# Kernel tuning notes

Measured on AMD Instinct MI355X. Metric: run time of the kernel, lower is better.

## Reference

```python
import jax, jax.numpy as jnp
import numpy as np


def _mlp(h, weights, biases, n_relu):
    # Linear(+ReLU) stack; ReLU on the first n_relu layers, final layer linear only.
    for i, (w, b) in enumerate(zip(weights, biases)):
        h = h @ w + b
        if i < n_relu:
            h = jax.nn.relu(h)
    return h


def setup_inputs() -> dict:
    key = jax.random.key(0)
    ks = jax.random.split(key, 12)
    B, M, E = 16384, 512, 1024

    def lin(k, fan_in, fan_out):
        # xavier-ish scaling so activations stay well-conditioned
        return jax.random.normal(k, (fan_in, fan_out), jnp.float32) * (1.0 / np.sqrt(fan_in))

    return {
        "x": jax.random.normal(ks[0], (B, M), jnp.float32),
        "rand_noise": jax.random.uniform(ks[1], (B, M), jnp.float32),
        "u_random": jax.random.uniform(ks[2], (B, M), jnp.float32),
        "marginals_min": jnp.zeros((M,), jnp.float32),
        "marginals_max": jnp.ones((M,), jnp.float32),
        "enc_w0": lin(ks[3], M, E), "enc_b0": jnp.full((E,), 0.01, jnp.float32),
        "enc_w1": lin(ks[4], E, E), "enc_b1": jnp.full((E,), 0.01, jnp.float32),
        "enc_w2": lin(ks[5], E, E), "enc_b2": jnp.full((E,), 0.01, jnp.float32),
        "enc_w3": lin(ks[6], E, E), "enc_b3": jnp.full((E,), 0.01, jnp.float32),
        "head_w0": lin(ks[7], E, E), "head_b0": jnp.full((E,), 0.01, jnp.float32),
        "head_w1": lin(ks[8], E, E), "head_b1": jnp.full((E,), 0.01, jnp.float32),
        "corruption_len": 307,
    }


def reference(x, rand_noise, u_random, marginals_min, marginals_max,
              enc_w0, enc_b0, enc_w1, enc_b1, enc_w2, enc_b2, enc_w3, enc_b3,
              head_w0, head_b0, head_w1, head_b1, corruption_len):
    B, M = x.shape
    # Vectorized equivalent of per-row randperm(m)[:corruption_len]:
    # top-k of iid uniform noise picks a uniform random subset of size k per row.
    _, idx = jax.lax.top_k(rand_noise, corruption_len)            # [B, k]
    mask = jnp.zeros((B, M), bool).at[jnp.arange(B)[:, None], idx].set(True)

    # Marginal samples ~ Uniform(min, max) per feature.
    x_random = marginals_min + u_random * (marginals_max - marginals_min)
    x_corrupted = jnp.where(mask, x_random, x)

    enc_ws = [enc_w0, enc_w1, enc_w2, enc_w3]
    enc_bs = [enc_b0, enc_b1, enc_b2, enc_b3]
    head_ws = [head_w0, head_w1]
    head_bs = [head_b0, head_b1]

    # Run both branches through one batched pass (same math, fewer launches).
    both = jnp.concatenate([x, x_corrupted], axis=0)              # [2B, M]
    h = _mlp(both, enc_ws, enc_bs, n_relu=3)                      # encoder depth 4
    h = _mlp(h, head_ws, head_bs, n_relu=1)                       # head depth 2
    embeddings, embeddings_corrupted = h[:B], h[B:]
    return embeddings, embeddings_corrupted
```

## Files before the change

### kernel.cpp

```cpp
#include <hip/hip_runtime.h>

typedef _Float16 f16x8 __attribute__((ext_vector_type(8)));
typedef float f32x4 __attribute__((ext_vector_type(4)));

__device__ __forceinline__ void gload16(const void* g, void* l) {
  __builtin_amdgcn_global_load_lds(
      (const __attribute__((address_space(1))) void*)g,
      (__attribute__((address_space(3))) void*)l, 16, 0, 0);
}

__device__ __forceinline__ void barfence() {
  asm volatile("" ::: "memory");
  __builtin_amdgcn_s_barrier();
  asm volatile("" ::: "memory");
}

__device__ __forceinline__ int xcd_swz(int orig, int nwg) {
  int q = nwg >> 3, r = nwg & 7;
  int x = orig & 7, loc = orig >> 3;
  int base = (x < r) ? x * (q + 1) : r * (q + 1) + (x - r) * q;
  return base + loc;
}

struct WPtrs { const float* w[6]; _Float16* wt[6]; };
__global__ __launch_bounds__(256) void transpose_all(WPtrs p) {
  const int N = 1024;
  __shared__ float tile[32][33];
  int y = blockIdx.y, layer, ky;
  if (y < 16) { layer = 0; ky = y; }
  else { int t = y - 16; layer = 1 + (t >> 5); ky = t & 31; }
  int K = (layer == 0) ? 512 : 1024;
  const float* W = p.w[layer];
  _Float16* WT = p.wt[layer];
  int tx = threadIdx.x, ty = threadIdx.y;
  int n0 = blockIdx.x * 32, k0 = ky * 32;
#pragma unroll
  for (int i = 0; i < 4; i++)
    tile[ty + i * 8][tx] = W[(long)(k0 + ty + i * 8) * N + (n0 + tx)];
  __syncthreads();
#pragma unroll
  for (int i = 0; i < 4; i++)
    WT[(long)(n0 + ty + i * 8) * K + (k0 + tx)] = (_Float16)tile[tx][ty + i * 8];
}

__global__ __launch_bounds__(256) void cast_f16(const float* __restrict__ in,
                                                _Float16* __restrict__ out, long n) {
  long i = ((long)blockIdx.x * 256 + threadIdx.x) * 4;
  if (i < n) {
    float4 v = *(const float4*)(in + i);
    typedef _Float16 f16x4 __attribute__((ext_vector_type(4)));
    f16x4 o = {(_Float16)v.x, (_Float16)v.y, (_Float16)v.z, (_Float16)v.w};
    *(f16x4*)(out + i) = o;
  }
}

__global__ __launch_bounds__(256) void topk_corrupt(
    const float* __restrict__ noise, const float* __restrict__ x,
    const float* __restrict__ u, const float* __restrict__ mmin,
    const float* __restrict__ mmax, const int* __restrict__ kptr,
    _Float16* __restrict__ dplain, _Float16* __restrict__ dcorr,
    int xrow0, int nrows) {
  int lane = threadIdx.x & 63;
  int r = (blockIdx.x << 2) + (threadIdx.x >> 6);
  if (r >= nrows) return;
  long row = (long)xrow0 + r;
  long rb = row * 512 + lane * 8;
  float4 n0 = *(const float4*)(noise + rb);
  float4 n1 = *(const float4*)(noise + rb + 4);
  unsigned v[8] = {__float_as_uint(n0.x), __float_as_uint(n0.y),
                   __float_as_uint(n0.z), __float_as_uint(n0.w),
                   __float_as_uint(n1.x), __float_as_uint(n1.y),
                   __float_as_uint(n1.z), __float_as_uint(n1.w)};
  int kk = *kptr;
  unsigned T = 0;
  for (int bit = 30; bit >= 0; --bit) {
    unsigned Tp = T | (1u << bit);
    int c = 0;
#pragma unroll
    for (int j = 0; j < 8; j++) c += (int)__popcll(__ballot(v[j] >= Tp));
    if (c >= kk) T = Tp;
  }
  int cgt = 0;
  unsigned long long eqb[8];
#pragma unroll
  for (int j = 0; j < 8; j++) {
    cgt += (int)__popcll(__ballot(v[j] > T));
    eqb[j] = __ballot(v[j] == T);
  }
  int need = kk - cgt;
  unsigned long long below = (1ull << lane) - 1ull;
  int rank_base = 0;
#pragma unroll
  for (int j = 0; j < 8; j++) rank_base += (int)__popcll(eqb[j] & below);

  float4 x0 = *(const float4*)(x + rb);
  float4 x1 = *(const float4*)(x + rb + 4);
  float4 u0 = *(const float4*)(u + rb);
  float4 u1 = *(const float4*)(u + rb + 4);
  int col = lane * 8;
  float4 mn0 = *(const float4*)(mmin + col);
  float4 mn1 = *(const float4*)(mmin + col + 4);
  float4 mx0 = *(const float4*)(mmax + col);
  float4 mx1 = *(const float4*)(mmax + col + 4);
  float xs[8] = {x0.x, x0.y, x0.z, x0.w, x1.x, x1.y, x1.z, x1.w};
  float us[8] = {u0.x, u0.y, u0.z, u0.w, u1.x, u1.y, u1.z, u1.w};
  float mns[8] = {mn0.x, mn0.y, mn0.z, mn0.w, mn1.x, mn1.y, mn1.z, mn1.w};
  float mxs[8] = {mx0.x, mx0.y, mx0.z, mx0.w, mx1.x, mx1.y, mx1.z, mx1.w};

  f16x8 po, co;
  int loc = 0;
#pragma unroll
  for (int j = 0; j < 8; j++) {
    bool eq = (v[j] == T);
    int rank = rank_base + loc;
    bool m = (v[j] > T) || (eq && (rank < need));
    loc += eq ? 1 : 0;
    float rv = mns[j] + us[j] * (mxs[j] - mns[j]);
    float cv = m ? rv : xs[j];
    po[j] = (_Float16)xs[j];
    co[j] = (_Float16)cv;
  }
  long ob = (long)r * 512 + lane * 8;
  if (dplain) *(f16x8*)(dplain + ob) = po;
  *(f16x8*)(dcorr + ob) = co;
}

template <bool RELU, bool OUTF32>
__global__ __launch_bounds__(512, 2) void gemm8p(const _Float16* __restrict__ A,
                                                 const _Float16* __restrict__ BT,
                                                 const float* __restrict__ bias,
                                                 void* __restrict__ Cout, int K) {
  const int N = 1024;
  __shared__ _Float16 S[2][4][8192];
  int tid = threadIdx.x;
  int lane = tid & 63, wave = tid >> 6;
  int wr = wave >> 2, wc = wave & 3;
  int logical = xcd_swz(blockIdx.x, gridDim.x);
  long arow0 = (long)(logical >> 2) * 256;
  int bcol0 = (logical & 3) * 256;

  int srow = tid >> 3;
  int scg = (tid & 7) ^ (srow & 7);
  const _Float16* gA[2][2];
  const _Float16* gB[2][2];
#pragma unroll
  for (int h = 0; h < 2; h++)
#pragma unroll
    for (int j = 0; j < 2; j++) {
      gA[h][j] = A + (arow0 + h * 128 + j * 64 + srow) * (long)K + scg * 8;
      gB[h][j] = BT + (long)(bcol0 + h * 128 + j * 64 + srow) * K + scg * 8;
    }
  int lo = tid * 8;

#define STG_A(BUF, H, T)                                   \
  do {                                                     \
    gload16(gA[H][0] + (T) * 64, &S[BUF][H][lo]);          \
    gload16(gA[H][1] + (T) * 64, &S[BUF][H][4096 + lo]);   \
  } while (0)
#define STG_B(BUF, H, T)                                      \
  do {                                                        \
    gload16(gB[H][0] + (T) * 64, &S[BUF][2 + H][lo]);         \
    gload16(gB[H][1] + (T) * 64, &S[BUF][2 + H][4096 + lo]);  \
  } while (0)

  int lr = lane & 15, g = lane >> 4, e = lr & 7;
  int cs0 = ((0 * 4 + g) ^ e) * 8;
  int cs1 = ((1 * 4 + g) ^ e) * 8;
  int aoff[4], boff[2];
#pragma unroll
  for (int mf = 0; mf < 4; mf++) aoff[mf] = (wr * 64 + mf * 16 + lr) * 64;
#pragma unroll
  for (int nf = 0; nf < 2; nf++) boff[nf] = (wc * 32 + nf * 16 + lr) * 64;

  f16x8 af0[4][2], af1[4][2];
  f16x8 bf0[2][2], bf1[2][2];
  f32x4 acc[2][2][4][2] = {};

#define LDA(DST, BUF, MQ)                                            \
  do {                                                               \
    _Pragma("unroll") for (int mf = 0; mf < 4; mf++) {               \
      DST[mf][0] = *(const f16x8*)&S[BUF][MQ][aoff[mf] + cs0];       \
      DST[mf][1] = *(const f16x8*)&S[BUF][MQ][aoff[mf] + cs1];       \
    }                                                                \
  } while (0)
#define LDB(DST, BUF, NQ)                                            \
  do {                                                               \
    _Pragma("unroll") for (int nf = 0; nf < 2; nf++) {               \
      DST[nf][0] = *(const f16x8*)&S[BUF][2 + NQ][boff[nf] + cs0];   \
      DST[nf][1] = *(const f16x8*)&S[BUF][2 + NQ][boff[nf] + cs1];   \
    }                                                                \
  } while (0)
#define MFMA_Q(AF, BF, MQ, NQ)                                       \
  do {                                                               \
    __builtin_amdgcn_s_setprio(1);                                   \
    _Pragma("unroll") for (int mf = 0; mf < 4; mf++)                 \
    _Pragma("unroll") for (int nf = 0; nf < 2; nf++)                 \
    _Pragma("unroll") for (int kk = 0; kk < 2; kk++)                 \
      acc[MQ][NQ][mf][nf] = __builtin_amdgcn_mfma_f32_16x16x32_f16(  \
          AF[mf][kk], BF[nf][kk], acc[MQ][NQ][mf][nf], 0, 0, 0);     \
    __builtin_amdgcn_s_setprio(0);                                   \
  } while (0)

  int NT = K / 64;
  STG_B(0, 0, 0); STG_B(0, 1, 0); STG_A(0, 0, 0); STG_A(0, 1, 0);
  asm volatile("s_waitcnt vmcnt(2)" ::: "memory");
  barfence();
  LDA(af0, 0, 0);
  LDB(bf1, 0, 1);

  for (int t = 0; t < NT; ++t) {
    int buf = t & 1, nbuf = buf ^ 1;
    LDB(bf0, buf, 0);
    if (t + 1 < NT) { STG_B(nbuf, 0, t + 1); STG_B(nbuf, 1, t + 1); }
    MFMA_Q(af0, bf0, 0, 0);
    if (t + 1 < NT) asm volatile("s_waitcnt vmcnt(4)" ::: "memory");
    else            asm volatile("s_waitcnt vmcnt(0)" ::: "memory");
    barfence();
    LDA(af1, buf, 1);
    if (t + 1 < NT) { STG_A(nbuf, 0, t + 1); STG_A(nbuf, 1, t + 1); }
    MFMA_Q(af0, bf1, 0, 1);
    MFMA_Q(af1, bf1, 1, 1);
    if (t + 1 < NT) asm volatile("s_waitcnt vmcnt(2)" ::: "memory");
    barfence();
    if (t + 1 < NT) { LDA(af0, nbuf, 0); LDB(bf1, nbuf, 1); }
    MFMA_Q(af1, bf0, 1, 0);
    if (t + 1 < NT) barfence();
  }
#undef STG_A
#undef STG_B
#undef LDA
#undef LDB
#undef MFMA_Q

  int r0 = (lane >> 4) * 4;
  float bv[2][2];
#pragma unroll
  for (int nq = 0; nq < 2; nq++)
#pragma unroll
    for (int nf = 0; nf < 2; nf++)
      bv[nq][nf] = bias[bcol0 + nq * 128 + wc * 32 + nf * 16 + lr];
#pragma unroll
  for (int mq = 0; mq < 2; mq++)
#pragma unroll
    for (int mf = 0; mf < 4; mf++) {
      long rowb = arow0 + mq * 128 + wr * 64 + mf * 16 + r0;
#pragma unroll
      for (int nq = 0; nq < 2; nq++)
#pragma unroll
        for (int nf = 0; nf < 2; nf++) {
          int col = bcol0 + nq * 128 + wc * 32 + nf * 16 + lr;
#pragma unroll
          for (int rr = 0; rr < 4; rr++) {
            float v = acc[mq][nq][mf][nf][rr] + bv[nq][nf];
            if (RELU) v = fmaxf(v, 0.f);
            if (OUTF32) ((float*)Cout)[(rowb + rr) * N + col] = v;
            else ((_Float16*)Cout)[(rowb + rr) * N + col] = (_Float16)v;
          }
        }
    }
}

extern "C" void kernel_launch(void* const* d_in, const int* in_sizes, int n_in,
                              void* d_out, int out_size, void* d_ws, size_t ws_size,
                              hipStream_t stream) {
  const float* x    = (const float*)d_in[0];
  const float* rn   = (const float*)d_in[1];
  const float* ur   = (const float*)d_in[2];
  const float* mmin = (const float*)d_in[3];
  const float* mmax = (const float*)d_in[4];
  const float* W[6]  = {(const float*)d_in[5],  (const float*)d_in[7],  (const float*)d_in[9],
                        (const float*)d_in[11], (const float*)d_in[13], (const float*)d_in[15]};
  const float* Bi[6] = {(const float*)d_in[6],  (const float*)d_in[8],  (const float*)d_in[10],
                        (const float*)d_in[12], (const float*)d_in[14], (const float*)d_in[16]};
  const int* kptr = (const int*)d_in[17];
  float* out = (float*)d_out;

  const long B = 16384;
  const int E = 1024;
  const int Ks[6] = {512, 1024, 1024, 1024, 1024, 1024};

  char* ws = (char*)d_ws;
  _Float16* wT[6];
  size_t off = 0;
  for (int i = 0; i < 6; i++) { wT[i] = (_Float16*)(ws + off); off += (size_t)Ks[i] * E * 2; }
  size_t rem = (ws_size > off) ? ws_size - off : 0;
  long R = 32768;
  while (R > 256 && (size_t)R * 5120 > rem) R >>= 1;

  _Float16* bothc = (_Float16*)(ws + off);
  _Float16* h0 = bothc + R * 512;
  _Float16* h1 = h0 + R * 1024;

  WPtrs wp;
  for (int i = 0; i < 6; i++) { wp.w[i] = W[i]; wp.wt[i] = wT[i]; }
  transpose_all<<<dim3(E / 32, 16 + 5 * 32), dim3(32, 8), 0, stream>>>(wp);

  for (long r0 = 0; r0 < 2 * B; r0 += R) {
    if (R == 2 * B) {
      topk_corrupt<<<dim3((unsigned)(B / 4)), dim3(256), 0, stream>>>(
          rn, x, ur, mmin, mmax, kptr, bothc, bothc + B * 512, 0, (int)B);
    } else {
      long plainEnd = (r0 < B) ? ((r0 + R < B) ? (r0 + R) : B) : r0;
      long p1 = plainEnd - r0;
      if (p1 > 0) {
        long n = p1 * 512;
        long blocks = (n / 4 + 255) / 256;
        cast_f16<<<dim3((unsigned)blocks), dim3(256), 0, stream>>>(x + r0 * 512, bothc, n);
      }
      long c0 = (r0 > B) ? r0 : B;
      long p2 = (r0 + R) - c0;
      if (p2 > 0) {
        topk_corrupt<<<dim3((unsigned)((p2 + 3) / 4)), dim3(256), 0, stream>>>(
            rn, x, ur, mmin, mmax, kptr, (_Float16*)nullptr,
            bothc + (c0 - r0) * 512, (int)(c0 - B), (int)p2);
      }
    }
    dim3 gg((unsigned)((R / 256) * 4)), gb(512);
    gemm8p<true,  false><<<gg, gb, 0, stream>>>(bothc, wT[0], Bi[0], (void*)h0, 512);
    gemm8p<true,  false><<<gg, gb, 0, stream>>>(h0,    wT[1], Bi[1], (void*)h1, 1024);
    gemm8p<true,  false><<<gg, gb, 0, stream>>>(h1,    wT[2], Bi[2], (void*)h0, 1024);
    gemm8p<false, false><<<gg, gb, 0, stream>>>(h0,    wT[3], Bi[3], (void*)h1, 1024);
    gemm8p<true,  false><<<gg, gb, 0, stream>>>(h1,    wT[4], Bi[4], (void*)h0, 1024);
    gemm8p<false, true ><<<gg, gb, 0, stream>>>(h0,    wT[5], Bi[5],
                                                 (void*)(out + r0 * 1024), 1024);
  }
}
```

Measured before the change: 405.5 us.

## Fuse weight transpose with top-k prep and use smaller-tile GEMM for final layer

Merges the weight transpose/cast and the top-k corruption into a single prep launch when the whole batch fits in workspace, removing one launch and letting the two independent jobs run on the GPU at the same time. Adds a new 128x128-tile GEMM with higher occupancy and nontemporal fp32 stores, used only for the final layer that writes the fp32 output. The smaller tile lowers reuse per block but may hide memory latency better on the write-heavy last layer.

```diff
diff --git a/kernel.cpp b/kernel.cpp
--- a/kernel.cpp
+++ b/kernel.cpp
@@ -23,47 +23,13 @@
 }
 
 struct WPtrs { const float* w[6]; _Float16* wt[6]; };
-__global__ __launch_bounds__(256) void transpose_all(WPtrs p) {
-  const int N = 1024;
-  __shared__ float tile[32][33];
-  int y = blockIdx.y, layer, ky;
-  if (y < 16) { layer = 0; ky = y; }
-  else { int t = y - 16; layer = 1 + (t >> 5); ky = t & 31; }
-  int K = (layer == 0) ? 512 : 1024;
-  const float* W = p.w[layer];
-  _Float16* WT = p.wt[layer];
-  int tx = threadIdx.x, ty = threadIdx.y;
-  int n0 = blockIdx.x * 32, k0 = ky * 32;
-#pragma unroll
-  for (int i = 0; i < 4; i++)
-    tile[ty + i * 8][tx] = W[(long)(k0 + ty + i * 8) * N + (n0 + tx)];
-  __syncthreads();
-#pragma unroll
-  for (int i = 0; i < 4; i++)
-    WT[(long)(n0 + ty + i * 8) * K + (k0 + tx)] = (_Float16)tile[tx][ty + i * 8];
-}
-
-__global__ __launch_bounds__(256) void cast_f16(const float* __restrict__ in,
-                                                _Float16* __restrict__ out, long n) {
-  long i = ((long)blockIdx.x * 256 + threadIdx.x) * 4;
-  if (i < n) {
-    float4 v = *(const float4*)(in + i);
-    typedef _Float16 f16x4 __attribute__((ext_vector_type(4)));
-    f16x4 o = {(_Float16)v.x, (_Float16)v.y, (_Float16)v.z, (_Float16)v.w};
-    *(f16x4*)(out + i) = o;
-  }
-}
-
-__global__ __launch_bounds__(256) void topk_corrupt(
+
+__device__ __forceinline__ void topk_row(
     const float* __restrict__ noise, const float* __restrict__ x,
     const float* __restrict__ u, const float* __restrict__ mmin,
-    const float* __restrict__ mmax, const int* __restrict__ kptr,
-    _Float16* __restrict__ dplain, _Float16* __restrict__ dcorr,
-    int xrow0, int nrows) {
+    const float* __restrict__ mmax, int kk, _Float16* __restrict__ dplain,
+    _Float16* __restrict__ dcorr, long row, long orow) {
   int lane = threadIdx.x & 63;
-  int r = (blockIdx.x << 2) + (threadIdx.x >> 6);
-  if (r >= nrows) return;
-  long row = (long)xrow0 + r;
   long rb = row * 512 + lane * 8;
   float4 n0 = *(const float4*)(noise + rb);
   float4 n1 = *(const float4*)(noise + rb + 4);
@@ -71,7 +37,6 @@
                    __float_as_uint(n0.z), __float_as_uint(n0.w),
                    __float_as_uint(n1.x), __float_as_uint(n1.y),
                    __float_as_uint(n1.z), __float_as_uint(n1.w)};
-  int kk = *kptr;
   unsigned T = 0;
   for (int bit = 30; bit >= 0; --bit) {
     unsigned Tp = T | (1u << bit);
@@ -120,9 +85,84 @@
     po[j] = (_Float16)xs[j];
     co[j] = (_Float16)cv;
   }
-  long ob = (long)r * 512 + lane * 8;
+  long ob = orow * 512 + lane * 8;
   if (dplain) *(f16x8*)(dplain + ob) = po;
   *(f16x8*)(dcorr + ob) = co;
+}
+
+__global__ __launch_bounds__(256) void prep_all(
+    const float* __restrict__ noise, const float* __restrict__ x,
+    const float* __restrict__ u, const float* __restrict__ mmin,
+    const float* __restrict__ mmax, const int* __restrict__ kptr,
+    _Float16* __restrict__ dplain, _Float16* __restrict__ dcorr,
+    WPtrs p, int ntopk) {
+  const int N = 1024;
+  if ((int)blockIdx.x < ntopk) {
+    int r = ((int)blockIdx.x << 2) + (threadIdx.x >> 6);
+    topk_row(noise, x, u, mmin, mmax, *kptr, dplain, dcorr, r, r);
+    return;
+  }
+  int b = (int)blockIdx.x - ntopk;
+  int bx = b & 31;
+  int y = b >> 5;
+  __shared__ float tile[32][33];
+  int layer, ky;
+  if (y < 16) { layer = 0; ky = y; }
+  else { int t = y - 16; layer = 1 + (t >> 5); ky = t & 31; }
+  int K = (layer == 0) ? 512 : 1024;
+  const float* W = p.w[layer];
+  _Float16* WT = p.wt[layer];
+  int tx = threadIdx.x & 31, ty = threadIdx.x >> 5;
+  int n0 = bx * 32, k0 = ky * 32;
+#pragma unroll
+  for (int i = 0; i < 4; i++)
+    tile[ty + i * 8][tx] = W[(long)(k0 + ty + i * 8) * N + (n0 + tx)];
+  __syncthreads();
+#pragma unroll
+  for (int i = 0; i < 4; i++)
+    WT[(long)(n0 + ty + i * 8) * K + (k0 + tx)] = (_Float16)tile[tx][ty + i * 8];
+}
+
+__global__ __launch_bounds__(256) void transpose_all(WPtrs p) {
+  const int N = 1024;
+  __shared__ float tile[32][33];
+  int y = blockIdx.y, layer, ky;
+  if (y < 16) { layer = 0; ky = y; }
+  else { int t = y - 16; layer = 1 + (t >> 5); ky = t & 31; }
+  int K = (layer == 0) ? 512 : 1024;
+  const float* W = p.w[layer];
+  _Float16* WT = p.wt[layer];
+  int tx = threadIdx.x, ty = threadIdx.y;
+  int n0 = blockIdx.x * 32, k0 = ky * 32;
+#pragma unroll
+  for (int i = 0; i < 4; i++)
+    tile[ty + i * 8][tx] = W[(long)(k0 + ty + i * 8) * N + (n0 + tx)];
+  __syncthreads();
+#pragma unroll
+  for (int i = 0; i < 4; i++)
+    WT[(long)(n0 + ty + i * 8) * K + (k0 + tx)] = (_Float16)tile[tx][ty + i * 8];
+}
+
+__global__ __launch_bounds__(256) void cast_f16(const float* __restrict__ in,
+                                                _Float16* __restrict__ out, long n) {
+  long i = ((long)blockIdx.x * 256 + threadIdx.x) * 4;
+  if (i < n) {
+    float4 v = *(const float4*)(in + i);
+    typedef _Float16 f16x4 __attribute__((ext_vector_type(4)));
+    f16x4 o = {(_Float16)v.x, (_Float16)v.y, (_Float16)v.z, (_Float16)v.w};
+    *(f16x4*)(out + i) = o;
+  }
+}
+
+__global__ __launch_bounds__(256) void topk_corrupt(
+    const float* __restrict__ noise, const float* __restrict__ x,
+    const float* __restrict__ u, const float* __restrict__ mmin,
+    const float* __restrict__ mmax, const int* __restrict__ kptr,
+    _Float16* __restrict__ dcorr, int xrow0, int nrows) {
+  int r = ((int)blockIdx.x << 2) + (threadIdx.x >> 6);
+  if (r >= nrows) return;
+  topk_row(noise, x, u, mmin, mmax, *kptr, (_Float16*)nullptr, dcorr,
+           (long)xrow0 + r, r);
 }
 
 template <bool RELU, bool OUTF32>
@@ -260,6 +300,110 @@
     }
 }
 
+template <bool RELU, bool OUTF32>
+__global__ __launch_bounds__(512, 4) void gemm2b(const _Float16* __restrict__ A,
+                                                 const _Float16* __restrict__ BT,
+                                                 const float* __restrict__ bias,
+                                                 void* __restrict__ Cout, int K) {
+  const int N = 1024;
+  __shared__ _Float16 S[2][2][8192];
+  int tid = threadIdx.x;
+  int lane = tid & 63, wave = tid >> 6;
+  int wr = wave >> 2, wc = wave & 3;
+  int logical = xcd_swz(blockIdx.x, gridDim.x);
+  long arow0 = (long)(logical >> 3) * 128;
+  int bcol0 = (logical & 7) * 128;
+
+  int srow = tid >> 3;
+  int scg = (tid & 7) ^ (srow & 7);
+  const _Float16* gA[2];
+  const _Float16* gB[2];
+#pragma unroll
+  for (int j = 0; j < 2; j++) {
+    gA[j] = A + (arow0 + j * 64 + srow) * (long)K + scg * 8;
+    gB[j] = BT + (long)(bcol0 + j * 64 + srow) * K + scg * 8;
+  }
+  int lo = tid * 8;
+
+#define STG(BUF, T)                                     \
+  do {                                                  \
+    gload16(gA[0] + (T) * 64, &S[BUF][0][lo]);          \
+    gload16(gA[1] + (T) * 64, &S[BUF][0][4096 + lo]);   \
+    gload16(gB[0] + (T) * 64, &S[BUF][1][lo]);          \
+    gload16(gB[1] + (T) * 64, &S[BUF][1][4096 + lo]);   \
+  } while (0)
+
+  int lr = lane & 15, g = lane >> 4, e = lr & 7;
+  int cs0 = ((0 * 4 + g) ^ e) * 8;
+  int cs1 = ((1 * 4 + g) ^ e) * 8;
+  int aoff[4], boff[2];
+#pragma unroll
+  for (int mf = 0; mf < 4; mf++) aoff[mf] = (wr * 64 + mf * 16 + lr) * 64;
+#pragma unroll
+  for (int nf = 0; nf < 2; nf++) boff[nf] = (wc * 32 + nf * 16 + lr) * 64;
+
+  f16x8 af[4][2], bf[2][2];
+  f32x4 acc[4][2] = {};
+
+  int NT = K / 64;
+  STG(0, 0);
+  asm volatile("s_waitcnt vmcnt(0)" ::: "memory");
+  barfence();
+
+  for (int t = 0; t < NT; ++t) {
+    int buf = t & 1, nbuf = buf ^ 1;
+    if (t + 1 < NT) STG(nbuf, t + 1);
+#pragma unroll
+    for (int mf = 0; mf < 4; mf++) {
+      af[mf][0] = *(const f16x8*)&S[buf][0][aoff[mf] + cs0];
+      af[mf][1] = *(const f16x8*)&S[buf][0][aoff[mf] + cs1];
+    }
+#pragma unroll
+    for (int nf = 0; nf < 2; nf++) {
+      bf[nf][0] = *(const f16x8*)&S[buf][1][boff[nf] + cs0];
+      bf[nf][1] = *(const f16x8*)&S[buf][1][boff[nf] + cs1];
+    }
+    __builtin_amdgcn_s_setprio(1);
+#pragma unroll
+    for (int mf = 0; mf < 4; mf++)
+#pragma unroll
+      for (int nf = 0; nf < 2; nf++)
+#pragma unroll
+        for (int kk = 0; kk < 2; kk++)
+          acc[mf][nf] = __builtin_amdgcn_mfma_f32_16x16x32_f16(
+              af[mf][kk], bf[nf][kk], acc[mf][nf], 0, 0, 0);
+    __builtin_amdgcn_s_setprio(0);
+    if (t + 1 < NT) {
+      asm volatile("s_waitcnt vmcnt(0)" ::: "memory");
+      barfence();
+    }
+  }
+#undef STG
+
+  int r0 = (lane >> 4) * 4;
+  float bv[2];
+#pragma unroll
+  for (int nf = 0; nf < 2; nf++) bv[nf] = bias[bcol0 + wc * 32 + nf * 16 + lr];
+#pragma unroll
+  for (int mf = 0; mf < 4; mf++) {
+    long rowb = arow0 + wr * 64 + mf * 16 + r0;
+#pragma unroll
+    for (int nf = 0; nf < 2; nf++) {
+      int col = bcol0 + wc * 32 + nf * 16 + lr;
+#pragma unroll
+      for (int rr = 0; rr < 4; rr++) {
+        float v = acc[mf][nf][rr] + bv[nf];
+        if (RELU) v = fmaxf(v, 0.f);
+        if (OUTF32) {
+          __builtin_nontemporal_store(v, &((float*)Cout)[(rowb + rr) * N + col]);
+        } else {
+          ((_Float16*)Cout)[(rowb + rr) * N + col] = (_Float16)v;
+        }
+      }
+    }
+  }
+}
+
 extern "C" void kernel_launch(void* const* d_in, const int* in_sizes, int n_in,
                               void* d_out, int out_size, void* d_ws, size_t ws_size,
                               hipStream_t stream) {
@@ -293,13 +437,23 @@
 
   WPtrs wp;
   for (int i = 0; i < 6; i++) { wp.w[i] = W[i]; wp.wt[i] = wT[i]; }
-  transpose_all<<<dim3(E / 32, 16 + 5 * 32), dim3(32, 8), 0, stream>>>(wp);
-
-  for (long r0 = 0; r0 < 2 * B; r0 += R) {
-    if (R == 2 * B) {
-      topk_corrupt<<<dim3((unsigned)(B / 4)), dim3(256), 0, stream>>>(
-          rn, x, ur, mmin, mmax, kptr, bothc, bothc + B * 512, 0, (int)B);
-    } else {
+
+  if (R == 2 * B) {
+    int ntopk = (int)(B / 4);
+    prep_all<<<dim3((unsigned)(ntopk + 32 * 176)), dim3(256), 0, stream>>>(
+        rn, x, ur, mmin, mmax, kptr, bothc, bothc + B * 512, wp, ntopk);
+
+    dim3 gg((unsigned)((R / 256) * 4)), gb(512);
+    dim3 gg2((unsigned)((R / 128) * 8));
+    gemm8p<true,  false><<<gg, gb, 0, stream>>>(bothc, wT[0], Bi[0], (void*)h0, 512);
+    gemm8p<true,  false><<<gg, gb, 0, stream>>>(h0,    wT[1], Bi[1], (void*)h1, 1024);
+    gemm8p<true,  false><<<gg, gb, 0, stream>>>(h1,    wT[2], Bi[2], (void*)h0, 1024);
+    gemm8p<false, false><<<gg, gb, 0, stream>>>(h0,    wT[3], Bi[3], (void*)h1, 1024);
+    gemm8p<true,  false><<<gg, gb, 0, stream>>>(h1,    wT[4], Bi[4], (void*)h0, 1024);
+    gemm2b<false, true ><<<gg2, gb, 0, stream>>>(h0,   wT[5], Bi[5], (void*)out, 1024);
+  } else {
+    transpose_all<<<dim3(E / 32, 16 + 5 * 32), dim3(32, 8), 0, stream>>>(wp);
+    for (long r0 = 0; r0 < 2 * B; r0 += R) {
       long plainEnd = (r0 < B) ? ((r0 + R < B) ? (r0 + R) : B) : r0;
       long p1 = plainEnd - r0;
       if (p1 > 0) {
@@ -311,17 +465,18 @@
       long p2 = (r0 + R) - c0;
       if (p2 > 0) {
         topk_corrupt<<<dim3((unsigned)((p2 + 3) / 4)), dim3(256), 0, stream>>>(
-            rn, x, ur, mmin, mmax, kptr, (_Float16*)nullptr,
-            bothc + (c0 - r0) * 512, (int)(c0 - B), (int)p2);
+            rn, x, ur, mmin, mmax, kptr, bothc + (c0 - r0) * 512,
+            (int)(c0 - B), (int)p2);
       }
-    }
-    dim3 gg((unsigned)((R / 256) * 4)), gb(512);
-    gemm8p<true,  false><<<gg, gb, 0, stream>>>(bothc, wT[0], Bi[0], (void*)h0, 512);
-    gemm8p<true,  false><<<gg, gb, 0, stream>>>(h0,    wT[1], Bi[1], (void*)h1, 1024);
-    gemm8p<true,  false><<<gg, gb, 0, stream>>>(h1,    wT[2], Bi[2], (void*)h0, 1024);
-    gemm8p<false, false><<<gg, gb, 0, stream>>>(h0,    wT[3], Bi[3], (void*)h1, 1024);
-    gemm8p<true,  false><<<gg, gb, 0, stream>>>(h1,    wT[4], Bi[4], (void*)h0, 1024);
-    gemm8p<false, true ><<<gg, gb, 0, stream>>>(h0,    wT[5], Bi[5],
-                                                 (void*)(out + r0 * 1024), 1024);
-  }
-}
+      dim3 gg((unsigned)((R / 256) * 4)), gb(512);
+      dim3 gg2((unsigned)((R / 128) * 8));
+      gemm8p<true,  false><<<gg, gb, 0, stream>>>(bothc, wT[0], Bi[0], (void*)h0, 512);
+      gemm8p<true,  false><<<gg, gb, 0, stream>>>(h0,    wT[1], Bi[1], (void*)h1, 1024);
+      gemm8p<true,  false><<<gg, gb, 0, stream>>>(h1,    wT[2], Bi[2], (void*)h0, 1024);
+      gemm8p<false, false><<<gg, gb, 0, stream>>>(h0,    wT[3], Bi[3], (void*)h1, 1024);
+      gemm8p<true,  false><<<gg, gb, 0, stream>>>(h1,    wT[4], Bi[4], (void*)h0, 1024);
+      gemm2b<false, true ><<<gg2, gb, 0, stream>>>(h0,   wT[5], Bi[5],
+                                                   (void*)(out + r0 * 1024), 1024);
+    }
+  }
+}
```

Result: no change. 404.5 us (median of 2 runs) (-0.3%).
